# Optimization experiments

Hardware: AMD Instinct MI355X
Metric: run time of the kernel (lower is better)

The kernel has to match this reference:

```python
import jax, jax.numpy as jnp
import numpy as np
import math

MIN_BITS, MAX_BITS = 4.0, 12.0
TARGET_RATE = 0.5
EPS = 1e-6


def setup_inputs() -> dict:
    key = jax.random.key(0)
    ks = jax.random.split(key, 9)
    B, C, H, W = 16, 256, 128, 128
    return {
        "features": jax.random.normal(ks[0], (B, C, H, W), dtype=jnp.float32),
        "conv1_w": jax.random.normal(ks[1], (16, 3), dtype=jnp.float32) * 0.3,
        "conv1_b": jax.random.normal(ks[2], (16,), dtype=jnp.float32) * 0.1,
        "conv2_w": jax.random.normal(ks[3], (1, 16), dtype=jnp.float32) * 0.3,
        "conv2_b": jax.random.normal(ks[4], (1,), dtype=jnp.float32) * 0.1,
        "lin1_w": jax.random.normal(ks[5], (32, 3), dtype=jnp.float32) * 0.3,
        "lin1_b": jax.random.normal(ks[6], (32,), dtype=jnp.float32) * 0.1,
        "lin2_w": jax.random.normal(ks[7], (1, 32), dtype=jnp.float32) * 0.3,
        "lin2_b": jax.random.normal(ks[8], (1,), dtype=jnp.float32) * 0.1,
        "snr_dB": 10,
    }


def reference(features, conv1_w, conv1_b, conv2_w, conv2_b,
              lin1_w, lin1_b, lin2_w, lin2_b, snr_dB):
    B, C, H, W = features.shape

    # ---- FIS_ImportanceAssessment: per-pixel channel statistics ----
    mean_sq = jnp.mean(features ** 2, axis=1, keepdims=True)          # (B,1,H,W)
    mean_abs = jnp.mean(jnp.abs(features), axis=1, keepdims=True)
    mag = jnp.sqrt(jnp.sum(features ** 2, axis=1, keepdims=True)) / math.sqrt(C)
    var = jnp.var(features, axis=1, keepdims=True, ddof=1)            # torch.var unbiased
    std = jnp.sqrt(var)                                               # torch.std unbiased
    var = var / (mean_sq + EPS)
    std = std / (mean_abs + EPS)
    mag = jnp.clip(mag, 0.0, 1.0)
    var = jnp.clip(var, 0.0, 1.0)
    std = jnp.clip(std, 0.0, 1.0)
    fuzzy = jnp.concatenate([mag, var, std], axis=1)                  # (B,3,H,W)

    # 1x1 conv fusion: 3 -> 16 -> 1
    h = jax.nn.relu(jnp.einsum('bchw,oc->bohw', fuzzy, conv1_w) + conv1_b[None, :, None, None])
    importance = jax.nn.sigmoid(
        jnp.einsum('bchw,oc->bohw', h, conv2_w) + conv2_b[None, :, None, None]
    )[:, 0]                                                           # (B,H,W)

    # ---- FIS_BitAllocation: tiny MLP 3 -> 32 -> 1 ----
    snr_norm = jnp.float32(snr_dB) / 30.0
    stacked = jnp.stack(
        [importance,
         jnp.full_like(importance, snr_norm),
         jnp.full_like(importance, TARGET_RATE)], axis=-1)            # (B,H,W,3)
    z = jax.nn.relu(jnp.einsum('bhwi,oi->bhwo', stacked, lin1_w) + lin1_b)
    b = jax.nn.sigmoid(jnp.einsum('bhwi,oi->bhwo', z, lin2_w) + lin2_b)[..., 0]
    bits = MIN_BITS + b * (MAX_BITS - MIN_BITS)                       # (B,H,W)

    # ---- AdaptiveQuantizer with STE ----
    levels = jnp.power(2.0, bits[:, None])                            # (B,1,H,W)
    f_min = jnp.min(features, axis=1, keepdims=True)
    f_max = jnp.max(features, axis=1, keepdims=True)
    denom = f_max - f_min + EPS
    f_norm = (features - f_min) / denom
    f_quant = jnp.round(f_norm * (levels - 1.0)) / (levels - 1.0)
    f_quant = f_norm + jax.lax.stop_gradient(f_quant - f_norm)        # STE
    quantized = f_quant * denom + f_min

    return quantized, importance, bits
```

## Files before the change

kernel.cpp:

```cpp
#include <hip/hip_runtime.h>
#include <math.h>

#define BB 16
#define CC 256
#define HH 128
#define WW 128
#define HW (HH*WW)
#define CHW (CC*HW)
#define NQ (BB*CHW)
#define NI (BB*HW)
#define PIX 64
#define NTHREADS 512
#define FEPS 1e-6f

__device__ __forceinline__ float quant_one(float x, float fmin, float denom, float lm1) {
    float fn = (x - fmin) / denom;
    float q  = rintf(fn * lm1) / lm1;
    return q * denom + fmin;
}

__global__ __launch_bounds__(NTHREADS, 4)
void hafis_fused(const float* __restrict__ feat,
                 const float* __restrict__ w1, const float* __restrict__ b1,
                 const float* __restrict__ w2, const float* __restrict__ b2,
                 const float* __restrict__ l1w, const float* __restrict__ l1b,
                 const float* __restrict__ l2w, const float* __restrict__ l2b,
                 const int*   __restrict__ snr_p,
                 float* __restrict__ out)
{
    __shared__ float tile[CC][PIX];
    __shared__ float pstat[5][8][PIX];
    __shared__ float4 params[PIX];

    const int t   = threadIdx.x;
    const int bid = blockIdx.x;
    const int w0  = (bid & 1) * PIX;
    const int h   = (bid >> 1) & (HH - 1);
    const int b   = bid >> 8;

    const float* base = feat + (size_t)b * CHW + (size_t)h * WW + w0;

    #pragma unroll
    for (int i = 0; i < (CC * PIX / 4) / NTHREADS; ++i) {
        int idx = i * NTHREADS + t;
        int c = idx >> 4;
        int v = (idx & 15) * 4;
        float4 val = *reinterpret_cast<const float4*>(base + (size_t)c * HW + v);
        *reinterpret_cast<float4*>(&tile[c][v]) = val;
    }
    __syncthreads();

    {
        int p   = t & 63;
        int sub = t >> 6;
        float s = 0.f, ss = 0.f, sa = 0.f;
        float mn = INFINITY, mx = -INFINITY;
        #pragma unroll
        for (int k = 0; k < CC / 8; ++k) {
            float x = tile[sub * (CC / 8) + k][p];
            s  += x;
            ss += x * x;
            sa += fabsf(x);
            mn = fminf(mn, x);
            mx = fmaxf(mx, x);
        }
        pstat[0][sub][p] = s;
        pstat[1][sub][p] = ss;
        pstat[2][sub][p] = sa;
        pstat[3][sub][p] = mn;
        pstat[4][sub][p] = mx;
    }
    __syncthreads();

    if (t < PIX) {
        int p = t;
        float s = 0.f, ss = 0.f, sa = 0.f, mn = INFINITY, mx = -INFINITY;
        #pragma unroll
        for (int sub = 0; sub < 8; ++sub) {
            s  += pstat[0][sub][p];
            ss += pstat[1][sub][p];
            sa += pstat[2][sub][p];
            mn = fminf(mn, pstat[3][sub][p]);
            mx = fmaxf(mx, pstat[4][sub][p]);
        }
        float mean_sq  = ss * (1.f / CC);
        float mean_abs = sa * (1.f / CC);
        float mag  = sqrtf(ss) * (1.f / 16.f);
        float var  = (ss - s * s * (1.f / CC)) * (1.f / (CC - 1));
        float stdv = sqrtf(var);
        float varn = var  / (mean_sq  + FEPS);
        float stdn = stdv / (mean_abs + FEPS);
        mag  = fminf(fmaxf(mag,  0.f), 1.f);
        varn = fminf(fmaxf(varn, 0.f), 1.f);
        stdn = fminf(fmaxf(stdn, 0.f), 1.f);

        float acc = b2[0];
        #pragma unroll
        for (int o = 0; o < 16; ++o) {
            float hh2 = w1[o * 3 + 0] * mag + w1[o * 3 + 1] * varn + w1[o * 3 + 2] * stdn + b1[o];
            hh2 = fmaxf(hh2, 0.f);
            acc += w2[o] * hh2;
        }
        float imp = 1.f / (1.f + expf(-acc));

        int iv = snr_p[0];
        float snr = (iv > -1000 && iv < 1000) ? (float)iv : __int_as_float(iv);
        float snrn = snr * (1.f / 30.f);
        float acc2 = l2b[0];
        #pragma unroll
        for (int o = 0; o < 32; ++o) {
            float z = l1w[o * 3 + 0] * imp + l1w[o * 3 + 1] * snrn + l1w[o * 3 + 2] * 0.5f + l1b[o];
            z = fmaxf(z, 0.f);
            acc2 += l2w[o] * z;
        }
        float bsig = 1.f / (1.f + expf(-acc2));
        float bits = 4.f + bsig * 8.f;
        float levels = exp2f(bits);
        float lm1 = levels - 1.f;
        float denom = mx - mn + FEPS;

        params[p] = make_float4(mn, denom, lm1, 0.f);

        size_t pix = (size_t)b * HW + (size_t)h * WW + w0 + p;
        out[NQ + pix]      = imp;
        out[NQ + NI + pix] = bits;
    }
    __syncthreads();

    {
        int pc   = t & 15;
        int crow = t >> 4;
        float4 pr0 = params[4 * pc + 0];
        float4 pr1 = params[4 * pc + 1];
        float4 pr2 = params[4 * pc + 2];
        float4 pr3 = params[4 * pc + 3];
        float* ob = out + (size_t)b * CHW + (size_t)h * WW + w0 + 4 * pc;
        #pragma unroll
        for (int k = 0; k < 8; ++k) {
            int c = crow + 32 * k;
            float4 x = *reinterpret_cast<const float4*>(&tile[c][4 * pc]);
            float4 r;
            r.x = quant_one(x.x, pr0.x, pr0.y, pr0.z);
            r.y = quant_one(x.y, pr1.x, pr1.y, pr1.z);
            r.z = quant_one(x.z, pr2.x, pr2.y, pr2.z);
            r.w = quant_one(x.w, pr3.x, pr3.y, pr3.z);
            *reinterpret_cast<float4*>(ob + (size_t)c * HW) = r;
        }
    }
}

extern "C" void kernel_launch(void* const* d_in, const int* in_sizes, int n_in,
                              void* d_out, int out_size, void* d_ws, size_t ws_size,
                              hipStream_t stream) {
    const float* feat = (const float*)d_in[0];
    const float* w1   = (const float*)d_in[1];
    const float* b1   = (const float*)d_in[2];
    const float* w2   = (const float*)d_in[3];
    const float* b2   = (const float*)d_in[4];
    const float* l1w  = (const float*)d_in[5];
    const float* l1b  = (const float*)d_in[6];
    const float* l2w  = (const float*)d_in[7];
    const float* l2b  = (const float*)d_in[8];
    const int*   snr  = (const int*)d_in[9];
    float* out = (float*)d_out;

    dim3 grid(BB * HH * (WW / PIX));
    dim3 block(NTHREADS);
    hipLaunchKernelGGL(hafis_fused, grid, block, 0, stream,
                       feat, w1, b1, w2, b2, l1w, l1b, l2w, l2b, snr, out);
}
```

Measured before the change: 461.0 us.

## Keep feature tile in registers, reduce with shuffles, use nontemporal stores

Each thread now keeps its eight float4 loads in registers instead of staging the 64 KB channel tile in LDS. Per-thread statistics are combined with cross-lane shuffles before a small LDS stage. The quantize step reuses the register data, replaces the final divide with a precomputed denom/lm1 scale, and writes output with nontemporal stores. Freeing LDS should allow more resident blocks and remove LDS traffic, at the cost of higher register pressure and slightly different rounding of the dequantized value.

```diff
diff --git a/kernel.cpp b/kernel.cpp
--- a/kernel.cpp
+++ b/kernel.cpp
@@ -13,10 +13,13 @@
 #define NTHREADS 512
 #define FEPS 1e-6f
 
-__device__ __forceinline__ float quant_one(float x, float fmin, float denom, float lm1) {
+typedef float f32x4 __attribute__((ext_vector_type(4)));
+
+__device__ __forceinline__ float quant_one(float x, float fmin, float denom,
+                                           float lm1, float scl) {
     float fn = (x - fmin) / denom;
-    float q  = rintf(fn * lm1) / lm1;
-    return q * denom + fmin;
+    float rq = rintf(fn * lm1);
+    return rq * scl + fmin;
 }
 
 __global__ __launch_bounds__(NTHREADS, 4)
@@ -28,8 +31,7 @@
                  const int*   __restrict__ snr_p,
                  float* __restrict__ out)
 {
-    __shared__ float tile[CC][PIX];
-    __shared__ float pstat[5][8][PIX];
+    __shared__ float pstat[8][5][4][16];
     __shared__ float4 params[PIX];
 
     const int t   = threadIdx.x;
@@ -38,55 +40,77 @@
     const int h   = (bid >> 1) & (HH - 1);
     const int b   = bid >> 8;
 
-    const float* base = feat + (size_t)b * CHW + (size_t)h * WW + w0;
+    const int g = t & 15;
+    const int r = t >> 4;
+
+    const size_t tilebase = (size_t)b * CHW + (size_t)h * WW + w0;
+    const float* src = feat + tilebase + (size_t)r * HW + 4 * g;
+
+    float4 d[8];
+    float s[4]  = {0.f, 0.f, 0.f, 0.f};
+    float ss[4] = {0.f, 0.f, 0.f, 0.f};
+    float sa[4] = {0.f, 0.f, 0.f, 0.f};
+    float mn[4] = {INFINITY, INFINITY, INFINITY, INFINITY};
+    float mx[4] = {-INFINITY, -INFINITY, -INFINITY, -INFINITY};
 
     #pragma unroll
-    for (int i = 0; i < (CC * PIX / 4) / NTHREADS; ++i) {
-        int idx = i * NTHREADS + t;
-        int c = idx >> 4;
-        int v = (idx & 15) * 4;
-        float4 val = *reinterpret_cast<const float4*>(base + (size_t)c * HW + v);
-        *reinterpret_cast<float4*>(&tile[c][v]) = val;
+    for (int i = 0; i < 8; ++i) {
+        float4 x = *reinterpret_cast<const float4*>(src + (size_t)i * 32 * HW);
+        d[i] = x;
+        const float* xs = reinterpret_cast<const float*>(&x);
+        #pragma unroll
+        for (int j = 0; j < 4; ++j) {
+            float v = xs[j];
+            s[j]  += v;
+            ss[j] += v * v;
+            sa[j] += fabsf(v);
+            mn[j] = fminf(mn[j], v);
+            mx[j] = fmaxf(mx[j], v);
+        }
     }
-    __syncthreads();
 
-    {
-        int p   = t & 63;
-        int sub = t >> 6;
-        float s = 0.f, ss = 0.f, sa = 0.f;
-        float mn = INFINITY, mx = -INFINITY;
+    #pragma unroll
+    for (int j = 0; j < 4; ++j) {
+        s[j]  += __shfl_xor(s[j], 16);  s[j]  += __shfl_xor(s[j], 32);
+        ss[j] += __shfl_xor(ss[j], 16); ss[j] += __shfl_xor(ss[j], 32);
+        sa[j] += __shfl_xor(sa[j], 16); sa[j] += __shfl_xor(sa[j], 32);
+        mn[j] = fminf(mn[j], __shfl_xor(mn[j], 16));
+        mn[j] = fminf(mn[j], __shfl_xor(mn[j], 32));
+        mx[j] = fmaxf(mx[j], __shfl_xor(mx[j], 16));
+        mx[j] = fmaxf(mx[j], __shfl_xor(mx[j], 32));
+    }
+
+    const int lane = t & 63;
+    const int wv   = t >> 6;
+    if (lane < 16) {
         #pragma unroll
-        for (int k = 0; k < CC / 8; ++k) {
-            float x = tile[sub * (CC / 8) + k][p];
-            s  += x;
-            ss += x * x;
-            sa += fabsf(x);
-            mn = fminf(mn, x);
-            mx = fmaxf(mx, x);
+        for (int j = 0; j < 4; ++j) {
+            pstat[wv][0][j][lane] = s[j];
+            pstat[wv][1][j][lane] = ss[j];
+            pstat[wv][2][j][lane] = sa[j];
+            pstat[wv][3][j][lane] = mn[j];
+            pstat[wv][4][j][lane] = mx[j];
         }
-        pstat[0][sub][p] = s;
-        pstat[1][sub][p] = ss;
-        pstat[2][sub][p] = sa;
-        pstat[3][sub][p] = mn;
-        pstat[4][sub][p] = mx;
     }
     __syncthreads();
 
     if (t < PIX) {
-        int p = t;
-        float s = 0.f, ss = 0.f, sa = 0.f, mn = INFINITY, mx = -INFINITY;
+        const int p  = t;
+        const int gg = p >> 2;
+        const int jj = p & 3;
+        float S = 0.f, SS = 0.f, SA = 0.f, MN = INFINITY, MX = -INFINITY;
         #pragma unroll
-        for (int sub = 0; sub < 8; ++sub) {
-            s  += pstat[0][sub][p];
-            ss += pstat[1][sub][p];
-            sa += pstat[2][sub][p];
-            mn = fminf(mn, pstat[3][sub][p]);
-            mx = fmaxf(mx, pstat[4][sub][p]);
+        for (int w = 0; w < 8; ++w) {
+            S  += pstat[w][0][jj][gg];
+            SS += pstat[w][1][jj][gg];
+            SA += pstat[w][2][jj][gg];
+            MN = fminf(MN, pstat[w][3][jj][gg]);
+            MX = fmaxf(MX, pstat[w][4][jj][gg]);
         }
-        float mean_sq  = ss * (1.f / CC);
-        float mean_abs = sa * (1.f / CC);
-        float mag  = sqrtf(ss) * (1.f / 16.f);
-        float var  = (ss - s * s * (1.f / CC)) * (1.f / (CC - 1));
+        float mean_sq  = SS * (1.f / CC);
+        float mean_abs = SA * (1.f / CC);
+        float mag  = sqrtf(SS) * (1.f / 16.f);
+        float var  = (SS - S * S * (1.f / CC)) * (1.f / (CC - 1));
         float stdv = sqrtf(var);
         float varn = var  / (mean_sq  + FEPS);
         float stdn = stdv / (mean_abs + FEPS);
@@ -97,7 +121,8 @@
         float acc = b2[0];
         #pragma unroll
         for (int o = 0; o < 16; ++o) {
-            float hh2 = w1[o * 3 + 0] * mag + w1[o * 3 + 1] * varn + w1[o * 3 + 2] * stdn + b1[o];
+            float hh2 = w1[o * 3 + 0] * mag + w1[o * 3 + 1] * varn
+                      + w1[o * 3 + 2] * stdn + b1[o];
             hh2 = fmaxf(hh2, 0.f);
             acc += w2[o] * hh2;
         }
@@ -109,17 +134,18 @@
         float acc2 = l2b[0];
         #pragma unroll
         for (int o = 0; o < 32; ++o) {
-            float z = l1w[o * 3 + 0] * imp + l1w[o * 3 + 1] * snrn + l1w[o * 3 + 2] * 0.5f + l1b[o];
+            float z = l1w[o * 3 + 0] * imp + l1w[o * 3 + 1] * snrn
+                    + l1w[o * 3 + 2] * 0.5f + l1b[o];
             z = fmaxf(z, 0.f);
             acc2 += l2w[o] * z;
         }
         float bsig = 1.f / (1.f + expf(-acc2));
         float bits = 4.f + bsig * 8.f;
-        float levels = exp2f(bits);
-        float lm1 = levels - 1.f;
-        float denom = mx - mn + FEPS;
+        float lm1  = exp2f(bits) - 1.f;
+        float denom = MX - MN + FEPS;
+        float scl   = denom / lm1;
 
-        params[p] = make_float4(mn, denom, lm1, 0.f);
+        params[p] = make_float4(MN, denom, lm1, scl);
 
         size_t pix = (size_t)b * HW + (size_t)h * WW + w0 + p;
         out[NQ + pix]      = imp;
@@ -127,25 +153,20 @@
     }
     __syncthreads();
 
-    {
-        int pc   = t & 15;
-        int crow = t >> 4;
-        float4 pr0 = params[4 * pc + 0];
-        float4 pr1 = params[4 * pc + 1];
-        float4 pr2 = params[4 * pc + 2];
-        float4 pr3 = params[4 * pc + 3];
-        float* ob = out + (size_t)b * CHW + (size_t)h * WW + w0 + 4 * pc;
-        #pragma unroll
-        for (int k = 0; k < 8; ++k) {
-            int c = crow + 32 * k;
-            float4 x = *reinterpret_cast<const float4*>(&tile[c][4 * pc]);
-            float4 r;
-            r.x = quant_one(x.x, pr0.x, pr0.y, pr0.z);
-            r.y = quant_one(x.y, pr1.x, pr1.y, pr1.z);
-            r.z = quant_one(x.z, pr2.x, pr2.y, pr2.z);
-            r.w = quant_one(x.w, pr3.x, pr3.y, pr3.z);
-            *reinterpret_cast<float4*>(ob + (size_t)c * HW) = r;
-        }
+    float4 pr0 = params[4 * g + 0];
+    float4 pr1 = params[4 * g + 1];
+    float4 pr2 = params[4 * g + 2];
+    float4 pr3 = params[4 * g + 3];
+    float* op = out + tilebase + (size_t)r * HW + 4 * g;
+    #pragma unroll
+    for (int i = 0; i < 8; ++i) {
+        float4 x = d[i];
+        f32x4 q;
+        q.x = quant_one(x.x, pr0.x, pr0.y, pr0.z, pr0.w);
+        q.y = quant_one(x.y, pr1.x, pr1.y, pr1.z, pr1.w);
+        q.z = quant_one(x.z, pr2.x, pr2.y, pr2.z, pr2.w);
+        q.w = quant_one(x.w, pr3.x, pr3.y, pr3.z, pr3.w);
+        __builtin_nontemporal_store(q, reinterpret_cast<f32x4*>(op + (size_t)i * 32 * HW));
     }
 }
 
```

After: 467.9 us. About the same (+1.5%).
